# Performance work log

Hardware: AMD Instinct MI355X
Metric: run time of the kernel (lower is better)

The kernel has to match this reference:

```python
import jax, jax.numpy as jnp
import numpy as np

B, LQ, LK = 16, 1024, 4096
QD, KD = 512, 512


def setup_inputs() -> dict:
    key = jax.random.key(0)
    ks = jax.random.split(key, 8)
    s = lambda d: 1.0 / np.sqrt(d)
    return {
        "query": jax.random.normal(ks[0], (B, LQ, QD), dtype=jnp.float32),
        "keys": jax.random.normal(ks[1], (B, LK, KD), dtype=jnp.float32),
        "Wq": jax.random.uniform(ks[2], (QD, KD), jnp.float32, -s(QD), s(QD)),
        "bq": jax.random.uniform(ks[3], (KD,), jnp.float32, -s(QD), s(QD)),
        "Wk": jax.random.uniform(ks[4], (KD, KD), jnp.float32, -s(KD), s(KD)),
        "bk": jax.random.uniform(ks[5], (KD,), jnp.float32, -s(KD), s(KD)),
        "Wv": jax.random.uniform(ks[6], (KD, KD), jnp.float32, -s(KD), s(KD)),
        "bv": jax.random.uniform(ks[7], (KD,), jnp.float32, -s(KD), s(KD)),
    }


def reference(query, keys, Wq, bq, Wk, bk, Wv, bv):
    scale = 1.0 / np.sqrt(KD)
    q = query @ Wq + bq                       # [B, LQ, KD]
    k = keys @ Wk + bk                        # [B, LK, KD]
    v = k @ Wv + bv                           # NOTE: value proj applied to projected keys (as in source)
    scores = jnp.einsum('bqd,bkd->bqk', q, k) * scale  # [B, LQ, LK]
    attn = jax.nn.softmax(scores, axis=2)
    context = jnp.einsum('bqk,bkd->bqd', attn, v)      # [B, LQ, KD]
    return context
```

## Files before the change

### kernel.cpp

```cpp
#include <hip/hip_runtime.h>
#include <hip/hip_bf16.h>
#include <stdint.h>


typedef __attribute__((ext_vector_type(8))) short bf16x8;
typedef __attribute__((ext_vector_type(4))) float f32x4;
typedef __attribute__((ext_vector_type(8))) unsigned short ushort8v;
typedef __attribute__((ext_vector_type(4))) unsigned short ushort4v;

__device__ __forceinline__ unsigned short f2bf(float f) {
  union { float f; unsigned int u; } x{f};
  unsigned int r = x.u + 0x7FFFu + ((x.u >> 16) & 1u);
  return (unsigned short)(r >> 16);
}
__device__ __forceinline__ float bf2f(unsigned short h) {
  union { unsigned int u; float f; } x{(unsigned int)h << 16};
  return x.f;
}

#define GLOAD_LDS16(gptr, lptr)                                                  \
  __builtin_amdgcn_global_load_lds((const __attribute__((address_space(1))) void*)(gptr), \
                                   (__attribute__((address_space(3))) void*)(lptr), 16, 0, 0)

__global__ __launch_bounds__(256) void cast_bf16_kernel(const float* __restrict__ in,
                                                        unsigned short* __restrict__ out,
                                                        long n) {
  long i = ((long)blockIdx.x * blockDim.x + threadIdx.x) * 8;
  long stride = (long)gridDim.x * blockDim.x * 8;
  for (; i < n; i += stride) {
    const float4* p = (const float4*)(in + i);
    float4 a = p[0], b = p[1];
    ushort8v o;
    o[0] = f2bf(a.x); o[1] = f2bf(a.y); o[2] = f2bf(a.z); o[3] = f2bf(a.w);
    o[4] = f2bf(b.x); o[5] = f2bf(b.y); o[6] = f2bf(b.z); o[7] = f2bf(b.w);
    *(ushort8v*)(out + i) = o;
  }
}

__global__ __launch_bounds__(256) void transpose_w_kernel(const float* __restrict__ W0,
                                                          const float* __restrict__ W1,
                                                          const float* __restrict__ W2,
                                                          unsigned short* __restrict__ T0,
                                                          unsigned short* __restrict__ T1,
                                                          unsigned short* __restrict__ T2) {
  const float* W = (blockIdx.z == 0) ? W0 : (blockIdx.z == 1) ? W1 : W2;
  unsigned short* T = (blockIdx.z == 0) ? T0 : (blockIdx.z == 1) ? T1 : T2;
  __shared__ float tile[32][33];
  int tx = threadIdx.x & 31, ty = threadIdx.x >> 5;
  int gx = blockIdx.x * 32 + tx;
  int gy0 = blockIdx.y * 32;
#pragma unroll
  for (int i = 0; i < 32; i += 8) tile[ty + i][tx] = W[(size_t)(gy0 + ty + i) * 512 + gx];
  __syncthreads();
  int ox = blockIdx.y * 32 + tx;
  int oy0 = blockIdx.x * 32;
#pragma unroll
  for (int i = 0; i < 32; i += 8)
    T[(size_t)(oy0 + ty + i) * 512 + ox] = f2bf(tile[tx][ty + i]);
}

template <int OUT_MODE, bool HAS_BIAS>
__global__ __launch_bounds__(256, 2) void gemm_nt(const unsigned short* __restrict__ A,
                                                  const unsigned short* __restrict__ Bt,
                                                  const float* __restrict__ bias,
                                                  void* __restrict__ Cout,
                                                  int M, int N, int K, float scale,
                                                  long sA, long sB, long sC) {
  __shared__ __align__(16) unsigned short lA[2][128][64];
  __shared__ __align__(16) unsigned short lB[2][128][64];
  const int tid = threadIdx.x;
  const int lane = tid & 63;
  const int wave = tid >> 6;
  const int z = blockIdx.z;
  const unsigned short* Ab = A + (size_t)z * sA;
  const unsigned short* Bb = Bt + (size_t)z * sB;
  const int m0 = blockIdx.y * 128;
  const int n0 = blockIdx.x * 128;

  f32x4 acc[4][4] = {};

  auto stage = [&](int buf, int kt) {
    const int k0 = kt * 64;
#pragma unroll
    for (int p = 0; p < 4; ++p) {
      int c = p * 4 + wave;
      int f = c * 512 + lane * 8;
      int row = f >> 6, col = f & 63;
      const unsigned short* gA = Ab + (size_t)(m0 + row) * K + (k0 + col);
      const unsigned short* gB = Bb + (size_t)(n0 + row) * K + (k0 + col);
      GLOAD_LDS16(gA, &lA[buf][0][0] + c * 512);
      GLOAD_LDS16(gB, &lB[buf][0][0] + c * 512);
    }
  };

  const int wm = wave >> 1, wn = wave & 1;
  const int lr = lane & 15;
  const int lk = (lane >> 4) << 3;

  const int KT = K >> 6;
  stage(0, 0);
  __syncthreads();
  int cur = 0;
  for (int kt = 0; kt < KT; ++kt) {
    if (kt + 1 < KT) stage(cur ^ 1, kt + 1);
#pragma unroll
    for (int kk = 0; kk < 64; kk += 32) {
      bf16x8 af[4], bfv[4];
#pragma unroll
      for (int i = 0; i < 4; ++i)
        af[i] = *(const bf16x8*)&lA[cur][wm * 64 + i * 16 + lr][kk + lk];
#pragma unroll
      for (int j = 0; j < 4; ++j)
        bfv[j] = *(const bf16x8*)&lB[cur][wn * 64 + j * 16 + lr][kk + lk];
#pragma unroll
      for (int i = 0; i < 4; ++i)
#pragma unroll
        for (int j = 0; j < 4; ++j)
          acc[i][j] = __builtin_amdgcn_mfma_f32_16x16x32_bf16(af[i], bfv[j], acc[i][j], 0, 0, 0);
    }
    __syncthreads();
    cur ^= 1;
  }

  const int ci = lane & 15;
  const int ri = (lane >> 4) * 4;
#pragma unroll
  for (int i = 0; i < 4; ++i) {
#pragma unroll
    for (int j = 0; j < 4; ++j) {
      int gm = m0 + wm * 64 + i * 16 + ri;
      int gn = n0 + wn * 64 + j * 16 + ci;
      float bv_ = HAS_BIAS ? bias[gn] : 0.f;
      f32x4 a = acc[i][j];
      if (OUT_MODE == 0) {
        unsigned short* C = (unsigned short*)Cout + (size_t)z * sC;
#pragma unroll
        for (int r = 0; r < 4; ++r)
          C[(size_t)(gm + r) * N + gn] = f2bf(a[r] * scale + bv_);
      } else if (OUT_MODE == 2) {
        float* C = (float*)Cout + (size_t)z * sC;
#pragma unroll
        for (int r = 0; r < 4; ++r)
          C[(size_t)(gm + r) * N + gn] = a[r] * scale + bv_;
      } else {
        unsigned short* C = (unsigned short*)Cout;
        int b_ = gm >> 12;
        int ml = gm & 4095;
        ushort4v pk;
#pragma unroll
        for (int r = 0; r < 4; ++r) pk[r] = f2bf(a[r] * scale + bv_);
        *(ushort4v*)&C[((size_t)b_ * 512 + gn) * 4096 + ml] = pk;
      }
    }
  }
}

__global__ __launch_bounds__(256) void softmax_kernel(unsigned short* __restrict__ s) {
  size_t row = blockIdx.x;
  unsigned short* p = s + row * 4096;
  int tid = threadIdx.x;
  int lane = tid & 63, wave = tid >> 6;

  ushort8v d0 = ((ushort8v*)p)[tid * 2];
  ushort8v d1 = ((ushort8v*)p)[tid * 2 + 1];
  float v[16];
#pragma unroll
  for (int j = 0; j < 8; ++j) { v[j] = bf2f(d0[j]); v[8 + j] = bf2f(d1[j]); }

  float m = v[0];
#pragma unroll
  for (int j = 1; j < 16; ++j) m = fmaxf(m, v[j]);
  for (int off = 32; off > 0; off >>= 1) m = fmaxf(m, __shfl_xor(m, off));
  __shared__ float redm[4], reds[4];
  if (lane == 0) redm[wave] = m;
  __syncthreads();
  m = fmaxf(fmaxf(redm[0], redm[1]), fmaxf(redm[2], redm[3]));

  float sum = 0.f;
#pragma unroll
  for (int j = 0; j < 16; ++j) { v[j] = __expf(v[j] - m); sum += v[j]; }
  for (int off = 32; off > 0; off >>= 1) sum += __shfl_xor(sum, off);
  if (lane == 0) reds[wave] = sum;
  __syncthreads();
  sum = reds[0] + reds[1] + reds[2] + reds[3];
  float r = 1.0f / sum;

#pragma unroll
  for (int j = 0; j < 8; ++j) { d0[j] = f2bf(v[j] * r); d1[j] = f2bf(v[8 + j] * r); }
  ((ushort8v*)p)[tid * 2] = d0;
  ((ushort8v*)p)[tid * 2 + 1] = d1;
}

extern "C" void kernel_launch(void* const* d_in, const int* in_sizes, int n_in,
                              void* d_out, int out_size, void* d_ws, size_t ws_size,
                              hipStream_t stream) {
  const float* query = (const float*)d_in[0];
  const float* keys  = (const float*)d_in[1];
  const float* Wq = (const float*)d_in[2];
  const float* bq = (const float*)d_in[3];
  const float* Wk = (const float*)d_in[4];
  const float* bk = (const float*)d_in[5];
  const float* Wv = (const float*)d_in[6];
  const float* bv = (const float*)d_in[7];
  float* out = (float*)d_out;

  char* w = (char*)d_ws;
  unsigned short* scores   = (unsigned short*)w;
  unsigned short* query_bf = (unsigned short*)w;
  unsigned short* keys_bf  = (unsigned short*)(w + 16777216);
  unsigned short* q_bf = (unsigned short*)(w + 134217728);
  unsigned short* k_bf = (unsigned short*)(w + 134217728 + 16777216);
  unsigned short* vT   = (unsigned short*)(w + 134217728 + 16777216 + 67108864);
  unsigned short* WqT  = (unsigned short*)(w + 285212672);
  unsigned short* WkT  = WqT + 262144;
  unsigned short* WvT  = WkT + 262144;

  const float scale = 0.04419417382415922f;

  cast_bf16_kernel<<<1024, 256, 0, stream>>>(query, query_bf, 8388608L);
  cast_bf16_kernel<<<2048, 256, 0, stream>>>(keys, keys_bf, 33554432L);
  transpose_w_kernel<<<dim3(16, 16, 3), 256, 0, stream>>>(Wq, Wk, Wv, WqT, WkT, WvT);

  gemm_nt<0, true><<<dim3(4, 128, 1), 256, 0, stream>>>(query_bf, WqT, bq, q_bf,
                                                        16384, 512, 512, 1.f, 0, 0, 0);
  gemm_nt<0, true><<<dim3(4, 512, 1), 256, 0, stream>>>(keys_bf, WkT, bk, k_bf,
                                                        65536, 512, 512, 1.f, 0, 0, 0);
  gemm_nt<1, true><<<dim3(4, 512, 1), 256, 0, stream>>>(k_bf, WvT, bv, vT,
                                                        65536, 512, 512, 1.f, 0, 0, 0);
  gemm_nt<0, false><<<dim3(32, 8, 16), 256, 0, stream>>>(q_bf, k_bf, nullptr, scores,
                                                         1024, 4096, 512, scale,
                                                         524288, 2097152, 4194304);
  softmax_kernel<<<16384, 256, 0, stream>>>(scores);
  gemm_nt<2, false><<<dim3(4, 8, 16), 256, 0, stream>>>(scores, vT, nullptr, out,
                                                        1024, 512, 4096, 1.f,
                                                        4194304, 2097152, 524288);
  (void)in_sizes; (void)n_in; (void)out_size; (void)ws_size;
}
```

Baseline: 708.8 us.

## Fuse QK^T, softmax and PV into a single flash-attention kernel

Replaces the score GEMM, the separate softmax pass and the PV GEMM with one flash-attention kernel. It keeps a 64-row Q tile in swizzled LDS, streams K tiles through double-buffered LDS, and uses an online softmax with running max and sum. The attention scale is folded into the Q projection epilogue. This removes the round trips of the 128MB bf16 score matrix through HBM, but launches only 256 blocks of 512 threads with heavy LDS use and block-wide syncs per tile. V is read directly from global memory without LDS staging.

```diff
diff --git a/kernel.cpp b/kernel.cpp
--- a/kernel.cpp
+++ b/kernel.cpp
@@ -59,21 +59,17 @@
     T[(size_t)(oy0 + ty + i) * 512 + ox] = f2bf(tile[tx][ty + i]);
 }
 
-template <int OUT_MODE, bool HAS_BIAS>
+template <int OUT_MODE>
 __global__ __launch_bounds__(256, 2) void gemm_nt(const unsigned short* __restrict__ A,
                                                   const unsigned short* __restrict__ Bt,
                                                   const float* __restrict__ bias,
                                                   void* __restrict__ Cout,
-                                                  int M, int N, int K, float scale,
-                                                  long sA, long sB, long sC) {
+                                                  int M, int N, int K, float scale) {
   __shared__ __align__(16) unsigned short lA[2][128][64];
   __shared__ __align__(16) unsigned short lB[2][128][64];
   const int tid = threadIdx.x;
   const int lane = tid & 63;
   const int wave = tid >> 6;
-  const int z = blockIdx.z;
-  const unsigned short* Ab = A + (size_t)z * sA;
-  const unsigned short* Bb = Bt + (size_t)z * sB;
   const int m0 = blockIdx.y * 128;
   const int n0 = blockIdx.x * 128;
 
@@ -86,8 +82,8 @@
       int c = p * 4 + wave;
       int f = c * 512 + lane * 8;
       int row = f >> 6, col = f & 63;
-      const unsigned short* gA = Ab + (size_t)(m0 + row) * K + (k0 + col);
-      const unsigned short* gB = Bb + (size_t)(n0 + row) * K + (k0 + col);
+      const unsigned short* gA = A + (size_t)(m0 + row) * K + (k0 + col);
+      const unsigned short* gB = Bt + (size_t)(n0 + row) * K + (k0 + col);
       GLOAD_LDS16(gA, &lA[buf][0][0] + c * 512);
       GLOAD_LDS16(gB, &lB[buf][0][0] + c * 512);
     }
@@ -130,65 +126,188 @@
     for (int j = 0; j < 4; ++j) {
       int gm = m0 + wm * 64 + i * 16 + ri;
       int gn = n0 + wn * 64 + j * 16 + ci;
-      float bv_ = HAS_BIAS ? bias[gn] : 0.f;
+      float bv_ = bias[gn];
       f32x4 a = acc[i][j];
       if (OUT_MODE == 0) {
-        unsigned short* C = (unsigned short*)Cout + (size_t)z * sC;
+        unsigned short* C = (unsigned short*)Cout;
 #pragma unroll
         for (int r = 0; r < 4; ++r)
-          C[(size_t)(gm + r) * N + gn] = f2bf(a[r] * scale + bv_);
-      } else if (OUT_MODE == 2) {
-        float* C = (float*)Cout + (size_t)z * sC;
-#pragma unroll
-        for (int r = 0; r < 4; ++r)
-          C[(size_t)(gm + r) * N + gn] = a[r] * scale + bv_;
+          C[(size_t)(gm + r) * N + gn] = f2bf((a[r] + bv_) * scale);
       } else {
         unsigned short* C = (unsigned short*)Cout;
         int b_ = gm >> 12;
         int ml = gm & 4095;
         ushort4v pk;
 #pragma unroll
-        for (int r = 0; r < 4; ++r) pk[r] = f2bf(a[r] * scale + bv_);
+        for (int r = 0; r < 4; ++r) pk[r] = f2bf((a[r] + bv_) * scale);
         *(ushort4v*)&C[((size_t)b_ * 512 + gn) * 4096 + ml] = pk;
       }
     }
   }
 }
 
-__global__ __launch_bounds__(256) void softmax_kernel(unsigned short* __restrict__ s) {
-  size_t row = blockIdx.x;
-  unsigned short* p = s + row * 4096;
-  int tid = threadIdx.x;
-  int lane = tid & 63, wave = tid >> 6;
-
-  ushort8v d0 = ((ushort8v*)p)[tid * 2];
-  ushort8v d1 = ((ushort8v*)p)[tid * 2 + 1];
-  float v[16];
-#pragma unroll
-  for (int j = 0; j < 8; ++j) { v[j] = bf2f(d0[j]); v[8 + j] = bf2f(d1[j]); }
-
-  float m = v[0];
-#pragma unroll
-  for (int j = 1; j < 16; ++j) m = fmaxf(m, v[j]);
-  for (int off = 32; off > 0; off >>= 1) m = fmaxf(m, __shfl_xor(m, off));
-  __shared__ float redm[4], reds[4];
-  if (lane == 0) redm[wave] = m;
+__global__ __launch_bounds__(512, 1) void flash_attn(const unsigned short* __restrict__ q,
+                                                     const unsigned short* __restrict__ k,
+                                                     const unsigned short* __restrict__ vT,
+                                                     float* __restrict__ out) {
+  __shared__ __align__(16) unsigned short lQ[64 * 512];
+  __shared__ __align__(16) unsigned short lK[2][128 * 64];
+  __shared__ __align__(16) unsigned short lP[64 * 128];
+  __shared__ float redm[64 * 8], reds[64 * 8];
+  __shared__ float m_s[64], rs_s[64];
+
+  const int tid = threadIdx.x;
+  const int lane = tid & 63;
+  const int w = tid >> 6;
+  const int bid = blockIdx.x;
+  const int b = (bid & 7) * 2 + ((bid >> 3) >> 4);
+  const int qt = (bid >> 3) & 15;
+
+  const unsigned short* Qb = q + ((size_t)b * 1024 + qt * 64) * 512;
+  const unsigned short* Kb = k + (size_t)b * 4096 * 512;
+  const unsigned short* Vb = vT + (size_t)b * 512 * 4096;
+
+  auto stageK = [&](int buf, int t2, int c2) {
+    const int kv0 = t2 * 128, kk = c2 * 64;
+#pragma unroll
+    for (int i = 0; i < 2; ++i) {
+      int byte = (i * 512 + tid) * 16;
+      int row = byte >> 7;
+      int colB = byte & 127;
+      int srcB = colB ^ ((row & 7) << 4);
+      GLOAD_LDS16(Kb + (size_t)(kv0 + row) * 512 + kk + (srcB >> 1),
+                  (char*)&lK[buf][0] + byte);
+    }
+  };
+
+#pragma unroll
+  for (int i = 0; i < 8; ++i) {
+    int byte = (i * 512 + tid) * 16;
+    int row = byte >> 10;
+    int colB = byte & 1023;
+    int srcB = (colB & ~127) | ((colB & 127) ^ ((row & 7) << 4));
+    GLOAD_LDS16(Qb + (size_t)row * 512 + (srcB >> 1), (char*)lQ + byte);
+  }
+  stageK(0, 0, 0);
+  float m_run = -1e30f, l_run = 0.f;
+  float rs_reg = 0.f;
   __syncthreads();
-  m = fmaxf(fmaxf(redm[0], redm[1]), fmaxf(redm[2], redm[3]));
-
-  float sum = 0.f;
-#pragma unroll
-  for (int j = 0; j < 16; ++j) { v[j] = __expf(v[j] - m); sum += v[j]; }
-  for (int off = 32; off > 0; off >>= 1) sum += __shfl_xor(sum, off);
-  if (lane == 0) reds[wave] = sum;
+
+  f32x4 acc_o[4][4] = {};
+  int cur = 0;
+
+  for (int t = 0; t < 32; ++t) {
+    f32x4 accS[4] = {};
+    for (int c = 0; c < 8; ++c) {
+      if (c < 7) stageK(cur ^ 1, t, c + 1);
+      else if (t < 31) stageK(cur ^ 1, t + 1, 0);
+      const int rowK = w * 16 + (lane & 15);
+#pragma unroll
+      for (int ks = 0; ks < 2; ++ks) {
+        int colKB = ((ks * 64 + ((lane >> 4) << 4)) ^ ((rowK & 7) << 4));
+        bf16x8 afK = *(const bf16x8*)((char*)&lK[cur][0] + rowK * 128 + colKB);
+#pragma unroll
+        for (int nf = 0; nf < 4; ++nf) {
+          int rowQ = nf * 16 + (lane & 15);
+          int colQB = c * 128 + ((ks * 64 + ((lane >> 4) << 4)) ^ ((rowQ & 7) << 4));
+          bf16x8 bfQ = *(const bf16x8*)((char*)lQ + rowQ * 1024 + colQB);
+          accS[nf] = __builtin_amdgcn_mfma_f32_16x16x32_bf16(afK, bfQ, accS[nf], 0, 0, 0);
+        }
+      }
+      __syncthreads();
+      cur ^= 1;
+    }
+
+#pragma unroll
+    for (int nf = 0; nf < 4; ++nf) {
+      f32x4 s = accS[nf];
+      float mx = fmaxf(fmaxf(s[0], s[1]), fmaxf(s[2], s[3]));
+      mx = fmaxf(mx, __shfl_xor(mx, 16));
+      mx = fmaxf(mx, __shfl_xor(mx, 32));
+      if (lane < 16) redm[(nf * 16 + lane) * 8 + w] = mx;
+    }
+    __syncthreads();
+    if (w == 0) {
+      f32x4 a = *(const f32x4*)&redm[lane * 8];
+      f32x4 a2 = *(const f32x4*)&redm[lane * 8 + 4];
+      float tmax = fmaxf(fmaxf(fmaxf(a[0], a[1]), fmaxf(a[2], a[3])),
+                         fmaxf(fmaxf(a2[0], a2[1]), fmaxf(a2[2], a2[3])));
+      float m_new = fmaxf(m_run, tmax);
+      rs_reg = __expf(m_run - m_new);
+      m_run = m_new;
+      m_s[lane] = m_new;
+      rs_s[lane] = rs_reg;
+    }
+    __syncthreads();
+#pragma unroll
+    for (int nf = 0; nf < 4; ++nf) {
+      int qrow = nf * 16 + (lane & 15);
+      float mq = m_s[qrow];
+      f32x4 s = accS[nf];
+      ushort4v pk;
+      float sum = 0.f;
+#pragma unroll
+      for (int r = 0; r < 4; ++r) {
+        float p = __expf(s[r] - mq);
+        sum += p;
+        pk[r] = f2bf(p);
+      }
+      sum += __shfl_xor(sum, 16);
+      sum += __shfl_xor(sum, 32);
+      if (lane < 16) reds[qrow * 8 + w] = sum;
+      int colB = (w * 32 + ((lane >> 4) << 3)) ^ ((qrow & 7) << 4);
+      *(ushort4v*)((char*)lP + qrow * 256 + colB) = pk;
+    }
+    __syncthreads();
+    if (w == 0) {
+      f32x4 a = *(const f32x4*)&reds[lane * 8];
+      f32x4 a2 = *(const f32x4*)&reds[lane * 8 + 4];
+      float tsum = (a[0] + a[1] + a[2] + a[3]) + (a2[0] + a2[1] + a2[2] + a2[3]);
+      l_run = l_run * rs_reg + tsum;
+    }
+#pragma unroll
+    for (int mf = 0; mf < 4; ++mf) {
+      f32x4 rsv = *(const f32x4*)&rs_s[(mf << 4) + ((lane >> 4) << 2)];
+#pragma unroll
+      for (int nf = 0; nf < 4; ++nf)
+#pragma unroll
+        for (int r = 0; r < 4; ++r) acc_o[mf][nf][r] *= rsv[r];
+    }
+#pragma unroll
+    for (int ks = 0; ks < 4; ++ks) {
+      bf16x8 bv_[4];
+#pragma unroll
+      for (int nf = 0; nf < 4; ++nf) {
+        int d = (w << 6) + (nf << 4) + (lane & 15);
+        bv_[nf] = *(const bf16x8*)(Vb + (size_t)d * 4096 + t * 128 + (ks << 5) + ((lane >> 4) << 3));
+      }
+#pragma unroll
+      for (int mf = 0; mf < 4; ++mf) {
+        int qr = (mf << 4) + (lane & 15);
+        int colB = ((ks << 6) + ((lane >> 4) << 4)) ^ ((qr & 7) << 4);
+        bf16x8 ap = *(const bf16x8*)((char*)lP + qr * 256 + colB);
+#pragma unroll
+        for (int nf = 0; nf < 4; ++nf)
+          acc_o[mf][nf] = __builtin_amdgcn_mfma_f32_16x16x32_bf16(ap, bv_[nf], acc_o[mf][nf], 0, 0, 0);
+      }
+    }
+  }
+
+  if (w == 0) rs_s[lane] = 1.f / l_run;
   __syncthreads();
-  sum = reds[0] + reds[1] + reds[2] + reds[3];
-  float r = 1.0f / sum;
-
-#pragma unroll
-  for (int j = 0; j < 8; ++j) { d0[j] = f2bf(v[j] * r); d1[j] = f2bf(v[8 + j] * r); }
-  ((ushort8v*)p)[tid * 2] = d0;
-  ((ushort8v*)p)[tid * 2 + 1] = d1;
+#pragma unroll
+  for (int mf = 0; mf < 4; ++mf) {
+    f32x4 il = *(const f32x4*)&rs_s[(mf << 4) + ((lane >> 4) << 2)];
+#pragma unroll
+    for (int nf = 0; nf < 4; ++nf) {
+      int d = (w << 6) + (nf << 4) + (lane & 15);
+#pragma unroll
+      for (int r = 0; r < 4; ++r) {
+        int qr = (mf << 4) + ((lane >> 4) << 2) + r;
+        out[((size_t)b * 1024 + qt * 64 + qr) * 512 + d] = acc_o[mf][nf][r] * il[r];
+      }
+    }
+  }
 }
 
 extern "C" void kernel_launch(void* const* d_in, const int* in_sizes, int n_in,
@@ -205,13 +324,12 @@
   float* out = (float*)d_out;
 
   char* w = (char*)d_ws;
-  unsigned short* scores   = (unsigned short*)w;
   unsigned short* query_bf = (unsigned short*)w;
   unsigned short* keys_bf  = (unsigned short*)(w + 16777216);
-  unsigned short* q_bf = (unsigned short*)(w + 134217728);
-  unsigned short* k_bf = (unsigned short*)(w + 134217728 + 16777216);
-  unsigned short* vT   = (unsigned short*)(w + 134217728 + 16777216 + 67108864);
-  unsigned short* WqT  = (unsigned short*)(w + 285212672);
+  unsigned short* q_bf = (unsigned short*)(w + 83886080);
+  unsigned short* k_bf = (unsigned short*)(w + 100663296);
+  unsigned short* vT   = (unsigned short*)(w + 167772160);
+  unsigned short* WqT  = (unsigned short*)(w + 234881024);
   unsigned short* WkT  = WqT + 262144;
   unsigned short* WvT  = WkT + 262144;
 
@@ -221,18 +339,13 @@
   cast_bf16_kernel<<<2048, 256, 0, stream>>>(keys, keys_bf, 33554432L);
   transpose_w_kernel<<<dim3(16, 16, 3), 256, 0, stream>>>(Wq, Wk, Wv, WqT, WkT, WvT);
 
-  gemm_nt<0, true><<<dim3(4, 128, 1), 256, 0, stream>>>(query_bf, WqT, bq, q_bf,
-                                                        16384, 512, 512, 1.f, 0, 0, 0);
-  gemm_nt<0, true><<<dim3(4, 512, 1), 256, 0, stream>>>(keys_bf, WkT, bk, k_bf,
-                                                        65536, 512, 512, 1.f, 0, 0, 0);
-  gemm_nt<1, true><<<dim3(4, 512, 1), 256, 0, stream>>>(k_bf, WvT, bv, vT,
-                                                        65536, 512, 512, 1.f, 0, 0, 0);
-  gemm_nt<0, false><<<dim3(32, 8, 16), 256, 0, stream>>>(q_bf, k_bf, nullptr, scores,
-                                                         1024, 4096, 512, scale,
-                                                         524288, 2097152, 4194304);
-  softmax_kernel<<<16384, 256, 0, stream>>>(scores);
-  gemm_nt<2, false><<<dim3(4, 8, 16), 256, 0, stream>>>(scores, vT, nullptr, out,
-                                                        1024, 512, 4096, 1.f,
-                                                        4194304, 2097152, 524288);
+  gemm_nt<0><<<dim3(4, 128), 256, 0, stream>>>(query_bf, WqT, bq, q_bf,
+                                               16384, 512, 512, scale);
+  gemm_nt<0><<<dim3(4, 512), 256, 0, stream>>>(keys_bf, WkT, bk, k_bf,
+                                               65536, 512, 512, 1.f);
+  gemm_nt<1><<<dim3(4, 512), 256, 0, stream>>>(k_bf, WvT, bv, vT,
+                                               65536, 512, 512, 1.f);
+  flash_attn<<<256, 512, 0, stream>>>(q_bf, k_bf, vT, out);
+
   (void)in_sizes; (void)n_in; (void)out_size; (void)ws_size;
 }
```

New measurement: 702.9 us. About the same (-0.8%).
